# Kernel tuning notes

Measured on AMD Instinct MI355X. Metric: run time of the kernel, lower is better.

Reference implementation:

```python
import jax, jax.numpy as jnp
import numpy as np


def setup_inputs() -> dict:
    key = jax.random.key(0)
    x = jax.random.normal(key, (4096, 4096), dtype=jnp.float32)
    return {"x": x}


def reference(x):
    """IDCT (DCT-III) along the last axis, scaled by 2 as in DREAMPlace:
        out[k] = x[0] + 2 * sum_{n=1}^{N-1} x[n] * cos(pi*n*(2k+1)/(2N))
    computed via a 2N-point FFT with twiddle-factor (expk) pre-multiply.
    """
    N = x.shape[-1]
    # twiddle expk[n] = exp(j*pi*n/(2N))
    theta = (jnp.pi / (2.0 * N)) * jnp.arange(N, dtype=jnp.float32)
    expk = jax.lax.complex(jnp.cos(theta), jnp.sin(theta))  # complex64 [N]
    c = x.astype(jnp.complex64) * expk                       # [M, N]
    # zero-pad to 2N; S[k] = sum_n c[n] exp(+j*2*pi*n*k/(2N)) = conj(fft(conj(c2)))[k]
    c2 = jnp.concatenate([c, jnp.zeros_like(c)], axis=-1)    # [M, 2N]
    S = jnp.fft.fft(jnp.conj(c2))                            # Re(S) == Re(2N*ifft(c2))
    # out[k] = 2*Re(S[k]) - x[0]
    y = 2.0 * jnp.real(S[..., :N]) - x[..., :1]
    return y.astype(x.dtype)
```

## Files before the change

### kernel.cpp

```cpp
#include <hip/hip_runtime.h>
#include <stdint.h>


#define Md 4096
#define Nfull 4096
#define Ph 2048
#define Kh 2048
#define BM 128
#define BN 128
#define BK 32
#define NKB 64
#define TILE 4096

typedef short bf16x8 __attribute__((ext_vector_type(8)));
typedef float floatx4 __attribute__((ext_vector_type(4)));
typedef unsigned short ushort_t;

__device__ __forceinline__ ushort_t f2bf(float f) {
  union { float f; uint32_t u; } v; v.f = f;
  uint32_t u = v.u;
  return (ushort_t)((u + 0x7fffu + ((u >> 16) & 1u)) >> 16);
}

__global__ __launch_bounds__(256) void prep_kernel(const float* __restrict__ x,
                                                   ushort_t* __restrict__ Ae,
                                                   ushort_t* __restrict__ Ao,
                                                   ushort_t* __restrict__ Ce,
                                                   ushort_t* __restrict__ Co) {
  int b = blockIdx.x;
  int t = threadIdx.x;
  if (b < 2048) {
    int bm = b >> 6, kb = b & 63;
    int r = t >> 1, h = t & 1;
    const float4* xp = (const float4*)(x + (((size_t)(bm * 128 + r)) << 12) + kb * 64 + h * 32);
    float4 v0 = xp[0], v1 = xp[1], v2 = xp[2], v3 = xp[3];
    float4 v4 = xp[4], v5 = xp[5], v6 = xp[6], v7 = xp[7];
    union { ushort_t us[8]; int4 v; } e0, e1, o0, o1;
    e0.us[0] = f2bf(v0.x); o0.us[0] = f2bf(v0.y);
    e0.us[1] = f2bf(v0.z); o0.us[1] = f2bf(v0.w);
    e0.us[2] = f2bf(v1.x); o0.us[2] = f2bf(v1.y);
    e0.us[3] = f2bf(v1.z); o0.us[3] = f2bf(v1.w);
    e0.us[4] = f2bf(v2.x); o0.us[4] = f2bf(v2.y);
    e0.us[5] = f2bf(v2.z); o0.us[5] = f2bf(v2.w);
    e0.us[6] = f2bf(v3.x); o0.us[6] = f2bf(v3.y);
    e0.us[7] = f2bf(v3.z); o0.us[7] = f2bf(v3.w);
    e1.us[0] = f2bf(v4.x); o1.us[0] = f2bf(v4.y);
    e1.us[1] = f2bf(v4.z); o1.us[1] = f2bf(v4.w);
    e1.us[2] = f2bf(v5.x); o1.us[2] = f2bf(v5.y);
    e1.us[3] = f2bf(v5.z); o1.us[3] = f2bf(v5.w);
    e1.us[4] = f2bf(v6.x); o1.us[4] = f2bf(v6.y);
    e1.us[5] = f2bf(v6.z); o1.us[5] = f2bf(v6.w);
    e1.us[6] = f2bf(v7.x); o1.us[6] = f2bf(v7.y);
    e1.us[7] = f2bf(v7.z); o1.us[7] = f2bf(v7.w);
    size_t tb = ((size_t)(bm * 64 + kb)) << 12;
    int c0 = (2 * h) * 1024 + r * 8;
    int c1 = c0 + 1024;
    *(int4*)(Ae + tb + c0) = e0.v;
    *(int4*)(Ae + tb + c1) = e1.v;
    *(int4*)(Ao + tb + c0) = o0.v;
    *(int4*)(Ao + tb + c1) = o1.v;
  } else {
    int b2 = b - 2048;
    int plane = b2 >> 10;
    int bn = (b2 & 1023) >> 6, kb = b2 & 63;
    ushort_t* T = plane ? Co : Ce;
    size_t tb = ((size_t)(bn * 64 + kb)) << 12;
    const float s = 3.14159265358979f / 8192.0f;
#pragma unroll
    for (int half = 0; half < 2; ++half) {
      int cc = t + half * 256;
      int g = cc >> 7, r = cc & 127;
      int p = bn * 128 + r;
      int tp = 2 * p + 1;
      int ni = kb * 32 + g * 8;
      union { ushort_t us[8]; int4 v; } pk;
#pragma unroll
      for (int jj = 0; jj < 8; ++jj) {
        int n = 2 * (ni + jj) + plane;
        int ang = (n * tp) & 16383;
        float c = (n == 0) ? 1.0f : 2.0f * __cosf(s * (float)ang);
        pk.us[jj] = f2bf(c);
      }
      *(int4*)(T + tb + cc * 8) = pk.v;
    }
  }
}

__global__ __launch_bounds__(256, 2) void gemm_fused(const ushort_t* __restrict__ Ae,
                                                     const ushort_t* __restrict__ Ao,
                                                     const ushort_t* __restrict__ Ce,
                                                     const ushort_t* __restrict__ Co,
                                                     float* __restrict__ out) {
  __shared__ __align__(16) ushort_t S0[16384];
  __shared__ __align__(16) ushort_t S1[16384];

  const int tid = threadIdx.x;
  const int wid = tid >> 6;
  const int lane = tid & 63;

  const int bm = blockIdx.y;
  const int bn = blockIdx.x;

  const int wm = (wid & 1) * 64;
  const int wn = (wid >> 1) * 64;
  const int lrow = lane & 15;

  floatx4 accE[4][4] = {};
  floatx4 accO[4][4] = {};

  const int lb = wid * 512;
  const ushort_t* pAe = Ae + (((size_t)bm * NKB) << 12) + (tid << 3);
  const ushort_t* pAo = Ao + (((size_t)bm * NKB) << 12) + (tid << 3);
  const ushort_t* pBe = Ce + (((size_t)bn * NKB) << 12) + (tid << 3);
  const ushort_t* pBo = Co + (((size_t)bn * NKB) << 12) + (tid << 3);

#define GLDS(src, dst) __builtin_amdgcn_global_load_lds( \
      (const __attribute__((address_space(1))) void*)(src), \
      (__attribute__((address_space(3))) void*)(dst), 16, 0, 0)

#define STAGE(SB, t) do { \
    size_t so_ = ((size_t)(t)) << 12; \
    _Pragma("unroll") \
    for (int i_ = 0; i_ < 2; ++i_) { \
      GLDS(pAe + so_ + i_ * 2048, SB + i_ * 2048 + lb); \
      GLDS(pAo + so_ + i_ * 2048, SB + 4096 + i_ * 2048 + lb); \
      GLDS(pBe + so_ + i_ * 2048, SB + 8192 + i_ * 2048 + lb); \
      GLDS(pBo + so_ + i_ * 2048, SB + 12288 + i_ * 2048 + lb); \
    } } while (0)

  const int g1024 = (lane >> 4) << 10;
  const int rb8 = lrow << 3;

#define COMPUTE(SB) do { \
    bf16x8 bE_[4], bO_[4]; \
    _Pragma("unroll") \
    for (int f_ = 0; f_ < 4; ++f_) { \
      int off_ = g1024 + rb8 + ((wn + f_ * 16) << 3); \
      bE_[f_] = *(const bf16x8*)(SB + 8192 + off_); \
      bO_[f_] = *(const bf16x8*)(SB + 12288 + off_); \
    } \
    __builtin_amdgcn_s_setprio(1); \
    _Pragma("unroll") \
    for (int im_ = 0; im_ < 4; ++im_) { \
      int off_ = g1024 + rb8 + ((wm + im_ * 16) << 3); \
      bf16x8 aE_ = *(const bf16x8*)(SB + off_); \
      bf16x8 aO_ = *(const bf16x8*)(SB + 4096 + off_); \
      _Pragma("unroll") \
      for (int jn_ = 0; jn_ < 4; ++jn_) { \
        accE[im_][jn_] = __builtin_amdgcn_mfma_f32_16x16x32_bf16(aE_, bE_[jn_], accE[im_][jn_], 0, 0, 0); \
        accO[im_][jn_] = __builtin_amdgcn_mfma_f32_16x16x32_bf16(aO_, bO_[jn_], accO[im_][jn_], 0, 0, 0); \
      } \
    } \
    __builtin_amdgcn_s_setprio(0); \
  } while (0)

#define WAITVM(n) do { \
    asm volatile("s_waitcnt vmcnt(" #n ")" ::: "memory"); \
    __builtin_amdgcn_sched_barrier(0); \
  } while (0)

  STAGE(S0, 0);
  STAGE(S1, 1);

  for (int t = 0; t < NKB - 4; t += 2) {
    WAITVM(8);
    __builtin_amdgcn_s_barrier();
    COMPUTE(S0);
    __builtin_amdgcn_s_barrier();
    STAGE(S0, t + 2);
    WAITVM(8);
    __builtin_amdgcn_s_barrier();
    COMPUTE(S1);
    __builtin_amdgcn_s_barrier();
    STAGE(S1, t + 3);
  }
  WAITVM(8);
  __builtin_amdgcn_s_barrier();
  COMPUTE(S0);
  __builtin_amdgcn_s_barrier();
  STAGE(S0, 62);
  WAITVM(8);
  __builtin_amdgcn_s_barrier();
  COMPUTE(S1);
  __builtin_amdgcn_s_barrier();
  STAGE(S1, 63);
  WAITVM(8);
  __builtin_amdgcn_s_barrier();
  COMPUTE(S0);
  WAITVM(0);
  __builtin_amdgcn_s_barrier();
  COMPUTE(S1);

#undef GLDS
#undef STAGE
#undef COMPUTE
#undef WAITVM

#pragma unroll
  for (int im = 0; im < 4; ++im) {
    int rb = bm * BM + wm + im * 16 + (lane >> 4) * 4;
#pragma unroll
    for (int jn = 0; jn < 4; ++jn) {
      int p = bn * BN + wn + jn * 16 + lrow;
      float* lo = out + (size_t)rb * Nfull + p;
      float* hi = out + (size_t)rb * Nfull + (Nfull - 1 - p);
#pragma unroll
      for (int r = 0; r < 4; ++r) {
        float e = accE[im][jn][r];
        float o = accO[im][jn][r];
        lo[(size_t)r * Nfull] = e + o;
        hi[(size_t)r * Nfull] = e - o;
      }
    }
  }
}

extern "C" void kernel_launch(void* const* d_in, const int* in_sizes, int n_in,
                              void* d_out, int out_size, void* d_ws, size_t ws_size,
                              hipStream_t stream) {
  const float* x = (const float*)d_in[0];
  float* out = (float*)d_out;
  ushort_t* Ae = (ushort_t*)d_ws;
  ushort_t* Ao = Ae + (size_t)8 * 1024 * 1024;
  ushort_t* Ce = Ao + (size_t)8 * 1024 * 1024;
  ushort_t* Co = Ce + (size_t)4 * 1024 * 1024;

  prep_kernel<<<4096, 256, 0, stream>>>(x, Ae, Ao, Ce, Co);

  dim3 grid(Ph / BN, Md / BM);
  gemm_fused<<<grid, 256, 0, stream>>>(Ae, Ao, Ce, Co, out);
}
```

Before: 180.0 us.

## Load B fragments directly from global into registers, bypassing LDS

Moves the cosine-matrix (B) operands out of the shared-memory staging path and into per-warp register double buffers loaded straight from global memory, and halves LDS allocation. This removes LDS writes/reads and bank traffic for B and may allow more resident blocks. In exchange, warps sharing the same B columns now fetch them redundantly from L2, register pressure rises, and waitcnt accounting is adjusted for the extra outstanding loads.

After: 186.6 us. 3.6% more time.

```diff
diff --git a/kernel.cpp b/kernel.cpp
--- a/kernel.cpp
+++ b/kernel.cpp
@@ -91,8 +91,8 @@
                                                      const ushort_t* __restrict__ Ce,
                                                      const ushort_t* __restrict__ Co,
                                                      float* __restrict__ out) {
-  __shared__ __align__(16) ushort_t S0[16384];
-  __shared__ __align__(16) ushort_t S1[16384];
+  __shared__ __align__(16) ushort_t S0[8192];
+  __shared__ __align__(16) ushort_t S1[8192];
 
   const int tid = threadIdx.x;
   const int wid = tid >> 6;
@@ -111,8 +111,12 @@
   const int lb = wid * 512;
   const ushort_t* pAe = Ae + (((size_t)bm * NKB) << 12) + (tid << 3);
   const ushort_t* pAo = Ao + (((size_t)bm * NKB) << 12) + (tid << 3);
-  const ushort_t* pBe = Ce + (((size_t)bn * NKB) << 12) + (tid << 3);
-  const ushort_t* pBo = Co + (((size_t)bn * NKB) << 12) + (tid << 3);
+
+  const int g1024 = (lane >> 4) << 10;
+  const int rb8 = lrow << 3;
+
+  const ushort_t* pBe = Ce + (((size_t)bn * NKB) << 12) + g1024 + rb8 + (wn << 3);
+  const ushort_t* pBo = Co + (((size_t)bn * NKB) << 12) + g1024 + rb8 + (wn << 3);
 
 #define GLDS(src, dst) __builtin_amdgcn_global_load_lds( \
       (const __attribute__((address_space(1))) void*)(src), \
@@ -120,25 +124,22 @@
 
 #define STAGE(SB, t) do { \
     size_t so_ = ((size_t)(t)) << 12; \
-    _Pragma("unroll") \
-    for (int i_ = 0; i_ < 2; ++i_) { \
-      GLDS(pAe + so_ + i_ * 2048, SB + i_ * 2048 + lb); \
-      GLDS(pAo + so_ + i_ * 2048, SB + 4096 + i_ * 2048 + lb); \
-      GLDS(pBe + so_ + i_ * 2048, SB + 8192 + i_ * 2048 + lb); \
-      GLDS(pBo + so_ + i_ * 2048, SB + 12288 + i_ * 2048 + lb); \
-    } } while (0)
-
-  const int g1024 = (lane >> 4) << 10;
-  const int rb8 = lrow << 3;
-
-#define COMPUTE(SB) do { \
-    bf16x8 bE_[4], bO_[4]; \
+    GLDS(pAe + so_, SB + lb); \
+    GLDS(pAe + so_ + 2048, SB + 2048 + lb); \
+    GLDS(pAo + so_, SB + 4096 + lb); \
+    GLDS(pAo + so_ + 2048, SB + 4096 + 2048 + lb); \
+  } while (0)
+
+#define BLOAD(bE_, bO_, t) do { \
+    const ushort_t* pe_ = pBe + (((size_t)(t)) << 12); \
+    const ushort_t* po_ = pBo + (((size_t)(t)) << 12); \
     _Pragma("unroll") \
     for (int f_ = 0; f_ < 4; ++f_) { \
-      int off_ = g1024 + rb8 + ((wn + f_ * 16) << 3); \
-      bE_[f_] = *(const bf16x8*)(SB + 8192 + off_); \
-      bO_[f_] = *(const bf16x8*)(SB + 12288 + off_); \
-    } \
+      bE_[f_] = *(const bf16x8*)(pe_ + f_ * 128); \
+      bO_[f_] = *(const bf16x8*)(po_ + f_ * 128); \
+    } } while (0)
+
+#define COMPUTE(SB, bE_, bO_) do { \
     __builtin_amdgcn_s_setprio(1); \
     _Pragma("unroll") \
     for (int im_ = 0; im_ < 4; ++im_) { \
@@ -159,40 +160,49 @@
     __builtin_amdgcn_sched_barrier(0); \
   } while (0)
 
+  bf16x8 bE0[4], bO0[4], bE1[4], bO1[4];
+
   STAGE(S0, 0);
+  BLOAD(bE0, bO0, 0);
   STAGE(S1, 1);
+  BLOAD(bE1, bO1, 1);
 
   for (int t = 0; t < NKB - 4; t += 2) {
-    WAITVM(8);
-    __builtin_amdgcn_s_barrier();
-    COMPUTE(S0);
+    WAITVM(12);
+    __builtin_amdgcn_s_barrier();
+    COMPUTE(S0, bE0, bO0);
     __builtin_amdgcn_s_barrier();
     STAGE(S0, t + 2);
-    WAITVM(8);
-    __builtin_amdgcn_s_barrier();
-    COMPUTE(S1);
+    BLOAD(bE0, bO0, t + 2);
+    WAITVM(12);
+    __builtin_amdgcn_s_barrier();
+    COMPUTE(S1, bE1, bO1);
     __builtin_amdgcn_s_barrier();
     STAGE(S1, t + 3);
+    BLOAD(bE1, bO1, t + 3);
   }
-  WAITVM(8);
-  __builtin_amdgcn_s_barrier();
-  COMPUTE(S0);
+  WAITVM(12);
+  __builtin_amdgcn_s_barrier();
+  COMPUTE(S0, bE0, bO0);
   __builtin_amdgcn_s_barrier();
   STAGE(S0, 62);
-  WAITVM(8);
-  __builtin_amdgcn_s_barrier();
-  COMPUTE(S1);
+  BLOAD(bE0, bO0, 62);
+  WAITVM(12);
+  __builtin_amdgcn_s_barrier();
+  COMPUTE(S1, bE1, bO1);
   __builtin_amdgcn_s_barrier();
   STAGE(S1, 63);
-  WAITVM(8);
-  __builtin_amdgcn_s_barrier();
-  COMPUTE(S0);
+  BLOAD(bE1, bO1, 63);
+  WAITVM(12);
+  __builtin_amdgcn_s_barrier();
+  COMPUTE(S0, bE0, bO0);
   WAITVM(0);
   __builtin_amdgcn_s_barrier();
-  COMPUTE(S1);
+  COMPUTE(S1, bE1, bO1);
 
 #undef GLDS
 #undef STAGE
+#undef BLOAD
 #undef COMPUTE
 #undef WAITVM
 
```
